# Optimization experiments

Hardware: AMD Instinct MI355X
Metric: run time of the kernel (lower is better)

## Reference

```python
import jax, jax.numpy as jnp
import numpy as np

N_NODES = 1_000_000
NODE_DIM = 128
HIDDEN_DIM = 64
NUM_SEGMENTS = 4096
NODE_SHIFT = 0.0
NODE_SCALE = 1.0


def setup_inputs() -> dict:
    key = jax.random.key(0)
    k_x, k_b, k_w1, k_b1, k_w2 = jax.random.split(key, 5)
    node_scalar = jax.random.normal(k_x, (N_NODES, NODE_DIM), dtype=jnp.float32)
    batch = jnp.sort(jax.random.randint(k_b, (N_NODES,), 0, NUM_SEGMENTS)).astype(jnp.int64)
    # nn.Linear default init: U(-1/sqrt(fan_in), 1/sqrt(fan_in)) for weight and bias
    lim1 = 1.0 / np.sqrt(NODE_DIM)
    w1 = jax.random.uniform(k_w1, (HIDDEN_DIM, NODE_DIM), minval=-lim1, maxval=lim1, dtype=jnp.float32)
    b1 = jax.random.uniform(k_b1, (HIDDEN_DIM,), minval=-lim1, maxval=lim1, dtype=jnp.float32)
    lim2 = 1.0 / np.sqrt(HIDDEN_DIM)
    w2 = jax.random.uniform(k_w2, (1, HIDDEN_DIM), minval=-lim2, maxval=lim2, dtype=jnp.float32) * NODE_SCALE
    b2 = jnp.full((1,), NODE_SHIFT, dtype=jnp.float32)  # nn.init.constant_(bias, node_shift)
    return {"node_scalar": node_scalar, "batch": batch, "w1": w1, "b1": b1, "w2": w2, "b2": b2}


def reference(node_scalar, batch, w1, b1, w2, b2):
    # node-wise MLP: Linear(128->64) -> SiLU -> Linear(64->1)
    h = jax.nn.silu(jnp.einsum('nd,hd->nh', node_scalar, w1) + b1)   # [N, 64]
    res = (jnp.einsum('nh,oh->no', h, w2) + b2).reshape(-1)          # [N]
    # scatter-sum over graph index
    out = jax.ops.segment_sum(res, batch, num_segments=NUM_SEGMENTS)  # [num_graphs]
    return out
```

## Files before the change

kernel.cpp:

```cpp
#include <hip/hip_runtime.h>
#include <hip/hip_bf16.h>


typedef __attribute__((ext_vector_type(8))) short bf16x8;
typedef __attribute__((ext_vector_type(4))) float f32x4;

__device__ __forceinline__ unsigned short f2bf(float f) {
    unsigned u = __float_as_uint(f);
    u += 0x7fffu + ((u >> 16) & 1u);
    return (unsigned short)(u >> 16);
}

__device__ __forceinline__ bf16x8 pack8(const float4 a, const float4 b) {
    bf16x8 r;
    r[0] = (short)f2bf(a.x); r[1] = (short)f2bf(a.y);
    r[2] = (short)f2bf(a.z); r[3] = (short)f2bf(a.w);
    r[4] = (short)f2bf(b.x); r[5] = (short)f2bf(b.y);
    r[6] = (short)f2bf(b.z); r[7] = (short)f2bf(b.w);
    return r;
}

__global__ void __launch_bounds__(256) scalar_out_mlp(
    const float* __restrict__ x, const int* __restrict__ batch,
    const float* __restrict__ w1, const float* __restrict__ b1,
    const float* __restrict__ w2, const float* __restrict__ b2,
    float* __restrict__ out, int n_nodes)
{
    const int tid  = threadIdx.x;
    const int wave = tid >> 6;
    const int l    = tid & 63;
    const int lr   = l & 15;
    const int lg   = l >> 4;

    bf16x8 wf[4][4];
#pragma unroll
    for (int t = 0; t < 4; ++t) {
        const float* wrow = w1 + (t * 16 + lr) * 128;
#pragma unroll
        for (int c = 0; c < 4; ++c) {
            const float* p = wrow + c * 32 + lg * 8;
            float4 u0 = *reinterpret_cast<const float4*>(p);
            float4 u1 = *reinterpret_cast<const float4*>(p + 4);
            wf[t][c] = pack8(u0, u1);
        }
    }
    float b1v[4], w2v[4];
#pragma unroll
    for (int t = 0; t < 4; ++t) {
        b1v[t] = b1[t * 16 + lr];
        w2v[t] = w2[t * 16 + lr];
    }
    const float b2s = b2[0];

    const int ntiles      = n_nodes >> 4;
    const int waves_total = gridDim.x * 4;
    const int gwave       = blockIdx.x * 4 + wave;

    for (int tile = gwave; tile < ntiles; tile += waves_total) {
        const int r0 = tile << 4;
        const float* xrow = x + (size_t)(r0 + lr) * 128 + lg * 8;

        bf16x8 af[4];
#pragma unroll
        for (int c = 0; c < 4; ++c) {
            float4 u0 = *reinterpret_cast<const float4*>(xrow + c * 32);
            float4 u1 = *reinterpret_cast<const float4*>(xrow + c * 32 + 4);
            af[c] = pack8(u0, u1);
        }

        f32x4 acc[4];
#pragma unroll
        for (int t = 0; t < 4; ++t) acc[t] = (f32x4){0.f, 0.f, 0.f, 0.f};

#pragma unroll
        for (int c = 0; c < 4; ++c)
#pragma unroll
            for (int t = 0; t < 4; ++t)
                acc[t] = __builtin_amdgcn_mfma_f32_16x16x32_bf16(af[c], wf[t][c], acc[t], 0, 0, 0);

        float p[4];
#pragma unroll
        for (int j = 0; j < 4; ++j) {
            float s = 0.f;
#pragma unroll
            for (int t = 0; t < 4; ++t) {
                float h  = acc[t][j] + b1v[t];
                float sg = 1.f / (1.f + __expf(-h));
                s += h * sg * w2v[t];
            }
            p[j] = s;
        }
#pragma unroll
        for (int j = 0; j < 4; ++j) {
            p[j] += __shfl_xor(p[j], 1, 16);
            p[j] += __shfl_xor(p[j], 2, 16);
            p[j] += __shfl_xor(p[j], 4, 16);
            p[j] += __shfl_xor(p[j], 8, 16);
        }

        const int bfirst = batch[r0];
        const int blast  = batch[r0 + 15];
        if (bfirst == blast) {
            float s = (p[0] + p[1] + p[2] + p[3]) + 4.f * b2s;
            s += __shfl_xor(s, 16, 64);
            s += __shfl_xor(s, 32, 64);
            if (l == 0) atomicAdd(&out[bfirst], s);
        } else {
            if (lr < 4) {
                const int j = lr;
                const int n = r0 + lg * 4 + j;
                atomicAdd(&out[batch[n]], p[j] + b2s);
            }
        }
    }
}

extern "C" void kernel_launch(void* const* d_in, const int* in_sizes, int n_in,
                              void* d_out, int out_size, void* d_ws, size_t ws_size,
                              hipStream_t stream) {
    const float* x     = (const float*)d_in[0];
    const int*   batch = (const int*)d_in[1];
    const float* w1    = (const float*)d_in[2];
    const float* b1    = (const float*)d_in[3];
    const float* w2    = (const float*)d_in[4];
    const float* b2    = (const float*)d_in[5];
    float* out = (float*)d_out;

    const int n_nodes = in_sizes[0] / 128;

    hipMemsetAsync(d_out, 0, (size_t)out_size * sizeof(float), stream);

    const int nblk = 1024;
    hipLaunchKernelGGL(scalar_out_mlp, dim3(nblk), dim3(256), 0, stream,
                       x, batch, w1, b1, w2, b2, out, n_nodes);
}
```

Before: 695.6 us.

## Software-prefetch next tile of x, double grid size, use fast rcp

Each wave now loads the next tile's x rows into registers before computing on the current tile, and hoists the batch index loads earlier, so global-load latency overlaps the MFMA and SiLU work. The grid doubles to 2048 blocks so more waves are in flight. Float-to-bf16 conversion switches to the library intrinsic, and the sigmoid divide uses a hardware reciprocal. The prefetch buffer adds 32 VGPRs per thread, which may lower occupancy.

New measurement: 669.4 us. 1.04x faster.

```diff
diff --git a/kernel.cpp b/kernel.cpp
--- a/kernel.cpp
+++ b/kernel.cpp
@@ -6,9 +6,9 @@
 typedef __attribute__((ext_vector_type(4))) float f32x4;
 
 __device__ __forceinline__ unsigned short f2bf(float f) {
-    unsigned u = __float_as_uint(f);
-    u += 0x7fffu + ((u >> 16) & 1u);
-    return (unsigned short)(u >> 16);
+    __hip_bfloat16 h = __float2bfloat16(f);
+    union { __hip_bfloat16 b; unsigned short u; } c; c.b = h;
+    return c.u;
 }
 
 __device__ __forceinline__ bf16x8 pack8(const float4 a, const float4 b) {
@@ -39,9 +39,8 @@
 #pragma unroll
         for (int c = 0; c < 4; ++c) {
             const float* p = wrow + c * 32 + lg * 8;
-            float4 u0 = *reinterpret_cast<const float4*>(p);
-            float4 u1 = *reinterpret_cast<const float4*>(p + 4);
-            wf[t][c] = pack8(u0, u1);
+            wf[t][c] = pack8(*reinterpret_cast<const float4*>(p),
+                             *reinterpret_cast<const float4*>(p + 4));
         }
     }
     float b1v[4], w2v[4];
@@ -52,56 +51,71 @@
     }
     const float b2s = b2[0];
 
-    const int ntiles      = n_nodes >> 4;
-    const int waves_total = gridDim.x * 4;
-    const int gwave       = blockIdx.x * 4 + wave;
+    const int ntiles = n_nodes >> 4;
+    const int stride = gridDim.x * 4;
+    int tile = blockIdx.x * 4 + wave;
 
-    for (int tile = gwave; tile < ntiles; tile += waves_total) {
-        const int r0 = tile << 4;
-        const float* xrow = x + (size_t)(r0 + lr) * 128 + lg * 8;
+    float4 cur[8];
+    if (tile < ntiles) {
+        const float* p = x + (size_t)((tile << 4) + lr) * 128 + lg * 8;
+#pragma unroll
+        for (int c = 0; c < 4; ++c) {
+            cur[2 * c]     = *reinterpret_cast<const float4*>(p + c * 32);
+            cur[2 * c + 1] = *reinterpret_cast<const float4*>(p + c * 32 + 4);
+        }
+    }
+
+    while (tile < ntiles) {
+        const int nt = tile + stride;
+        float4 nxt[8];
+        if (nt < ntiles) {
+            const float* p = x + (size_t)((nt << 4) + lr) * 128 + lg * 8;
+#pragma unroll
+            for (int c = 0; c < 4; ++c) {
+                nxt[2 * c]     = *reinterpret_cast<const float4*>(p + c * 32);
+                nxt[2 * c + 1] = *reinterpret_cast<const float4*>(p + c * 32 + 4);
+            }
+        }
+
+        const int r0     = tile << 4;
+        const int bfirst = batch[r0];
+        const int blast  = batch[r0 + 15];
 
         bf16x8 af[4];
 #pragma unroll
-        for (int c = 0; c < 4; ++c) {
-            float4 u0 = *reinterpret_cast<const float4*>(xrow + c * 32);
-            float4 u1 = *reinterpret_cast<const float4*>(xrow + c * 32 + 4);
-            af[c] = pack8(u0, u1);
-        }
+        for (int c = 0; c < 4; ++c) af[c] = pack8(cur[2 * c], cur[2 * c + 1]);
 
         f32x4 acc[4];
 #pragma unroll
         for (int t = 0; t < 4; ++t) acc[t] = (f32x4){0.f, 0.f, 0.f, 0.f};
-
 #pragma unroll
         for (int c = 0; c < 4; ++c)
 #pragma unroll
             for (int t = 0; t < 4; ++t)
                 acc[t] = __builtin_amdgcn_mfma_f32_16x16x32_bf16(af[c], wf[t][c], acc[t], 0, 0, 0);
 
-        float p[4];
+        float p4[4];
 #pragma unroll
         for (int j = 0; j < 4; ++j) {
             float s = 0.f;
 #pragma unroll
             for (int t = 0; t < 4; ++t) {
                 float h  = acc[t][j] + b1v[t];
-                float sg = 1.f / (1.f + __expf(-h));
+                float sg = __builtin_amdgcn_rcpf(1.f + __expf(-h));
                 s += h * sg * w2v[t];
             }
-            p[j] = s;
+            p4[j] = s;
         }
 #pragma unroll
         for (int j = 0; j < 4; ++j) {
-            p[j] += __shfl_xor(p[j], 1, 16);
-            p[j] += __shfl_xor(p[j], 2, 16);
-            p[j] += __shfl_xor(p[j], 4, 16);
-            p[j] += __shfl_xor(p[j], 8, 16);
+            p4[j] += __shfl_xor(p4[j], 1, 16);
+            p4[j] += __shfl_xor(p4[j], 2, 16);
+            p4[j] += __shfl_xor(p4[j], 4, 16);
+            p4[j] += __shfl_xor(p4[j], 8, 16);
         }
 
-        const int bfirst = batch[r0];
-        const int blast  = batch[r0 + 15];
         if (bfirst == blast) {
-            float s = (p[0] + p[1] + p[2] + p[3]) + 4.f * b2s;
+            float s = (p4[0] + p4[1] + p4[2] + p4[3]) + 4.f * b2s;
             s += __shfl_xor(s, 16, 64);
             s += __shfl_xor(s, 32, 64);
             if (l == 0) atomicAdd(&out[bfirst], s);
@@ -109,9 +123,13 @@
             if (lr < 4) {
                 const int j = lr;
                 const int n = r0 + lg * 4 + j;
-                atomicAdd(&out[batch[n]], p[j] + b2s);
+                atomicAdd(&out[batch[n]], p4[j] + b2s);
             }
         }
+
+#pragma unroll
+        for (int i = 0; i < 8; ++i) cur[i] = nxt[i];
+        tile = nt;
     }
 }
 
@@ -130,7 +148,7 @@
 
     hipMemsetAsync(d_out, 0, (size_t)out_size * sizeof(float), stream);
 
-    const int nblk = 1024;
+    const int nblk = 2048;
     hipLaunchKernelGGL(scalar_out_mlp, dim3(nblk), dim3(256), 0, stream,
                        x, batch, w1, b1, w2, b2, out, n_nodes);
 }
```
